# Performance work log

Hardware: AMD Instinct MI355X
Metric: run time of the kernel (lower is better)

The kernel has to match this reference:

```python
import jax, jax.numpy as jnp
import numpy as np

NUM_HEADS = 4

def setup_inputs() -> dict:
    key = jax.random.key(0)
    k1, k2, k3, k4 = jax.random.split(key, 4)
    B, N, D = 8, 768, 2048
    x = jax.random.normal(k1, (B, N, D), dtype=jnp.float32)
    s = 1.0 / np.sqrt(N)
    W_qk = jax.random.normal(k2, (N, N), dtype=jnp.float32) * s
    W_v = jax.random.normal(k3, (N, N), dtype=jnp.float32) * s
    W_out = jax.random.normal(k4, (N, N), dtype=jnp.float32) * s
    return {"x": x, "W_qk": W_qk, "W_v": W_v, "W_out": W_out}

def reference(x, W_qk, W_v, W_out):
    B, N, D = x.shape
    H = NUM_HEADS
    n = N // H
    y = jnp.swapaxes(x, 1, 2)                    # (B, D, N): attention over channels D
    qk = y @ W_qk.T                              # (B, D, N)
    v = y @ W_v.T                                # (B, D, N)
    # to heads: (B, D, N) -> (B, H, D, n)
    qk = jnp.swapaxes(qk.reshape(B, D, H, n), 1, 2)
    v = jnp.swapaxes(v.reshape(B, D, H, n), 1, 2)
    dot = jnp.einsum('bhdn,bhen->bhde', qk, qk)  # (B, H, D, D)
    q2 = jnp.sum(qk * qk, axis=-1)               # (B, H, D)
    # negative squared Euclidean distance logits: 2*q.k - ||q||^2 - ||k||^2
    logits = 2.0 * dot - q2[..., :, None] - q2[..., None, :]
    attn = jax.nn.softmax(logits, axis=-1)
    w = jnp.einsum('bhde,bhen->bhdn', attn, v)   # (B, H, D, n)
    # from heads: (B, H, D, n) -> (B, D, N)
    w = jnp.swapaxes(w, 1, 2).reshape(B, D, N)
    out = w @ W_out.T                            # (B, D, N)
    return jnp.swapaxes(out, 1, 2)               # (B, N, D)
```

## Files before the change

### kernel.cpp

```cpp
#include <hip/hip_runtime.h>
#include <stdint.h>

#define B_  8
#define N_  768
#define D_  2048
#define H_  4
#define HN  192

#define QROW 200
#define VROW 72
#define KTILE_B 25600
#define VTILE_B 27648

#define LOG2E 1.4426950408889634f
#define C2    2.8853901617f

typedef unsigned short u16;
typedef float    f32x4 __attribute__((ext_vector_type(4)));
typedef __bf16   bf16x8 __attribute__((ext_vector_type(8)));
typedef __bf16   bf16x4 __attribute__((ext_vector_type(4)));
typedef uint32_t u32x4 __attribute__((ext_vector_type(4)));
typedef uint32_t u32x2 __attribute__((ext_vector_type(2)));

__device__ __forceinline__ u16 f2bf(float f) {
  return __builtin_bit_cast(u16, (__bf16)f);
}

typedef const __attribute__((address_space(1))) void* gas_ptr;
typedef __attribute__((address_space(3))) void* las_ptr;
__device__ __forceinline__ void gld16(const void* g, void* l) {
  __builtin_amdgcn_global_load_lds((gas_ptr)g, (las_ptr)l, 16, 0, 0);
}

__global__ __launch_bounds__(256) void transpose_x(const float* __restrict__ x,
                                                   u16* __restrict__ xt) {
  __shared__ float tile[64][65];
  const int d0 = blockIdx.x * 64;
  const int n0 = blockIdx.y * 64;
  const int b  = blockIdx.z;
  const int t   = threadIdx.x;
  const int col = t & 63;
  const int rb  = (t >> 6) * 16;
  const float* src = x + ((size_t)b * N_ + n0) * D_ + d0;
  #pragma unroll
  for (int i = 0; i < 16; i++)
    tile[rb + i][col] = src[(size_t)(rb + i) * D_ + col];
  __syncthreads();
  u16* dst = xt + ((size_t)b * D_ + d0) * N_ + n0;
  #pragma unroll
  for (int i = 0; i < 16; i++)
    dst[(size_t)(rb + i) * N_ + col] = f2bf(tile[col][rb + i]);
}

__global__ __launch_bounds__(256) void cvt_w(const float* __restrict__ a,
                                             const float* __restrict__ b,
                                             const float* __restrict__ c,
                                             u16* __restrict__ oa,
                                             u16* __restrict__ ob,
                                             u16* __restrict__ oc) {
  const float* src = (blockIdx.y == 0) ? a : ((blockIdx.y == 1) ? b : c);
  u16*         dst = (blockIdx.y == 0) ? oa : ((blockIdx.y == 1) ? ob : oc);
  const int i = (blockIdx.x * 256 + threadIdx.x) * 4;
  f32x4 v = *(const f32x4*)(src + i);
  u16 tmp[4];
  #pragma unroll
  for (int j = 0; j < 4; j++) tmp[j] = f2bf(v[j]);
  *(u32x2*)(dst + i) = *(u32x2*)tmp;
}

__global__ __launch_bounds__(256) void zero_q2(float* __restrict__ q2) {
  q2[blockIdx.x * 256 + threadIdx.x] = 0.f;
}

__global__ __launch_bounds__(256, 2) void qkv_gemm(const u16* __restrict__ xt,
                                                   const u16* __restrict__ wqk,
                                                   const u16* __restrict__ wv,
                                                   u16* __restrict__ qkb,
                                                   u16* __restrict__ vtb,
                                                   float* __restrict__ q2) {
  const int b     = blockIdx.z;
  const int dtile = blockIdx.x;
  const int d0    = dtile * 128;
  const int j0    = blockIdx.y * 128;
  const int tid  = threadIdx.x;
  const int wave = tid >> 6, lane = tid & 63;
  const int l15  = lane & 15, quad = lane >> 4;
  const int wm = wave >> 1, wn = wave & 1;

  __shared__ u16 At[128 * 32];
  __shared__ u16 Bq[128 * 32];
  __shared__ u16 Bv[128 * 32];

  const f32x4 fz = {0.f, 0.f, 0.f, 0.f};
  f32x4 accq[4][4];
  f32x4 accv[4][4];
  #pragma unroll
  for (int i = 0; i < 4; i++)
    #pragma unroll
    for (int j = 0; j < 4; j++) { accq[i][j] = fz; accv[i][j] = fz; }

  const int srow  = tid >> 2;
  const int sbyte = (tid & 3) * 16;
  const u16* ax = xt  + ((size_t)b * D_ + d0 + srow) * N_;
  const u16* bq = wqk + (size_t)(j0 + srow) * N_;
  const u16* bv = wv  + (size_t)(j0 + srow) * N_;

  for (int k0 = 0; k0 < N_; k0 += 32) {
    __syncthreads();
    #pragma unroll
    for (int c = 0; c < 2; c++) {
      gld16((const char*)(ax + (size_t)c * 64 * N_ + k0) + sbyte,
            (char*)At + c * 4096 + tid * 16);
      gld16((const char*)(bq + (size_t)c * 64 * N_ + k0) + sbyte,
            (char*)Bq + c * 4096 + tid * 16);
      gld16((const char*)(bv + (size_t)c * 64 * N_ + k0) + sbyte,
            (char*)Bv + c * 4096 + tid * 16);
    }
    __syncthreads();

    bf16x8 Af[4];
    #pragma unroll
    for (int mi = 0; mi < 4; mi++)
      Af[mi] = *(const bf16x8*)&At[(wm * 64 + mi * 16 + l15) * 32 + quad * 8];
    #pragma unroll
    for (int ni = 0; ni < 4; ni++) {
      bf16x8 Bqf = *(const bf16x8*)&Bq[(wn * 64 + ni * 16 + l15) * 32 + quad * 8];
      bf16x8 Bvf = *(const bf16x8*)&Bv[(wn * 64 + ni * 16 + l15) * 32 + quad * 8];
      #pragma unroll
      for (int mi = 0; mi < 4; mi++) {
        accq[ni][mi] = __builtin_amdgcn_mfma_f32_16x16x32_bf16(Bqf, Af[mi], accq[ni][mi], 0, 0, 0);
        accv[mi][ni] = __builtin_amdgcn_mfma_f32_16x16x32_bf16(Af[mi], Bvf, accv[mi][ni], 0, 0, 0);
      }
    }
  }

  const int h_w  = (j0 + wn * 64) / HN;
  const int jn_w = (j0 + wn * 64) % HN;
  const size_t bh = (size_t)b * H_ + h_w;

  #pragma unroll
  for (int md = 0; md < 4; md++) {
    float s = 0.f;
    #pragma unroll
    for (int nj = 0; nj < 4; nj++)
      #pragma unroll
      for (int r = 0; r < 4; r++) { float v = accq[nj][md][r]; s += v * v; }
    s += __shfl_xor(s, 16, 64);
    s += __shfl_xor(s, 32, 64);
    if (quad == 0)
      atomicAdd(&q2[bh * D_ + d0 + wm * 64 + md * 16 + l15], s * LOG2E);
  }

  u16* qtbase = qkb + bh * (size_t)(D_ * QROW);
  #pragma unroll
  for (int md = 0; md < 4; md++) {
    const size_t dro = (size_t)(d0 + wm * 64 + md * 16 + l15) * QROW;
    #pragma unroll
    for (int nj = 0; nj < 4; nj++) {
      bf16x4 tmp;
      #pragma unroll
      for (int r = 0; r < 4; r++) tmp[r] = (__bf16)accq[nj][md][r];
      *(bf16x4*)(qtbase + dro + jn_w + nj * 16 + quad * 4) = tmp;
    }
  }

  const int etile = dtile * 2 + wm;
  u16* vtbase = vtb + bh * (size_t)(32 * HN * VROW) + (size_t)etile * (HN * VROW);
  #pragma unroll
  for (int ni = 0; ni < 4; ni++) {
    const size_t jro = (size_t)(jn_w + ni * 16 + l15) * VROW;
    #pragma unroll
    for (int mi = 0; mi < 4; mi++) {
      bf16x4 tmp;
      #pragma unroll
      for (int r = 0; r < 4; r++) tmp[r] = (__bf16)accv[mi][ni][r];
      *(bf16x4*)(vtbase + jro + mi * 16 + quad * 4) = tmp;
    }
  }
}

__global__ __launch_bounds__(256, 2) void attn_kernel(const u16* __restrict__ qkb,
                                                      const u16* __restrict__ vtb,
                                                      const float* __restrict__ q2,
                                                      u16* __restrict__ wbuf) {
  const int bid  = blockIdx.x;
  const int bh   = (bid & 7) * 4 + (bid >> 7);
  const int dblk = (bid >> 3) & 15;
  const int b = bh >> 2, h = bh & 3;
  const int tid  = threadIdx.x;
  const int wave = tid >> 6, lane = tid & 63;
  const int l15  = lane & 15, quad = lane >> 4;

  __shared__ u16 Klds[64 * QROW];
  __shared__ u16 Vlds[HN * VROW];
  __shared__ u16 Plds[4][32][VROW];

  const u16* kg = qkb + (size_t)bh * (D_ * QROW);
  const u16* vg = vtb + (size_t)bh * (32 * HN * VROW);
  const float* q2g = q2 + (size_t)bh * D_;

  bf16x8 Qf[2][6];
  {
    const u16* qrow = kg + (size_t)(dblk * 128 + wave * 32 + l15) * QROW + quad * 8;
    #pragma unroll
    for (int nt = 0; nt < 2; nt++)
      #pragma unroll
      for (int f = 0; f < 6; f++)
        Qf[nt][f] = *(const bf16x8*)(qrow + (size_t)nt * 16 * QROW + f * 32);
  }
  float cd[2];
  cd[0] = q2g[dblk * 128 + wave * 32 + l15];
  cd[1] = q2g[dblk * 128 + wave * 32 + 16 + l15];

  bf16x8 OnesF;
  #pragma unroll
  for (int j = 0; j < 8; j++) OnesF[j] = (__bf16)1.0f;

  const f32x4 fz = {0.f, 0.f, 0.f, 0.f};
  f32x4 O[2][12];
  f32x4 Or[2];
  #pragma unroll
  for (int mt = 0; mt < 2; mt++) {
    Or[mt] = fz;
    #pragma unroll
    for (int c = 0; c < 12; c++) O[mt][c] = fz;
  }

  for (int t = 0; t < 32; t++) {
    __syncthreads();
    {
      const char* ks = (const char*)kg + (size_t)t * KTILE_B;
      char* kd = (char*)Klds;
      for (int c = wave; c < 25; c += 4)
        gld16(ks + c * 1024 + lane * 16, kd + c * 1024 + lane * 16);
      const char* vs = (const char*)vg + (size_t)t * VTILE_B;
      char* vd = (char*)Vlds;
      for (int c = wave; c < 27; c += 4)
        gld16(vs + c * 1024 + lane * 16, vd + c * 1024 + lane * 16);
    }
    __syncthreads();

    #pragma unroll
    for (int et = 0; et < 4; et++) {
      bf16x8 Kf[6];
      #pragma unroll
      for (int f = 0; f < 6; f++)
        Kf[f] = *(const bf16x8*)&Klds[(et * 16 + l15) * QROW + f * 32 + quad * 8];
      f32x4 S0 = fz, S1 = fz;
      __builtin_amdgcn_s_setprio(1);
      #pragma unroll
      for (int f = 0; f < 6; f++) {
        S0 = __builtin_amdgcn_mfma_f32_16x16x32_bf16(Kf[f], Qf[0][f], S0, 0, 0, 0);
        S1 = __builtin_amdgcn_mfma_f32_16x16x32_bf16(Kf[f], Qf[1][f], S1, 0, 0, 0);
      }
      __builtin_amdgcn_s_setprio(0);
      const f32x4 ce = *(const f32x4*)&q2g[t * 64 + et * 16 + quad * 4];
      bf16x4 pb0, pb1;
      #pragma unroll
      for (int r = 0; r < 4; r++) {
        float p0 = __builtin_amdgcn_exp2f(__builtin_fmaf(S0[r], C2, -(ce[r] + cd[0])));
        float p1 = __builtin_amdgcn_exp2f(__builtin_fmaf(S1[r], C2, -(ce[r] + cd[1])));
        pb0[r] = (__bf16)p0;
        pb1[r] = (__bf16)p1;
      }
      *(bf16x4*)&Plds[wave][l15][et * 16 + quad * 4]      = pb0;
      *(bf16x4*)&Plds[wave][16 + l15][et * 16 + quad * 4] = pb1;
    }

    #pragma unroll
    for (int kk = 0; kk < 2; kk++) {
      bf16x8 Pf0 = *(const bf16x8*)&Plds[wave][l15][kk * 32 + quad * 8];
      bf16x8 Pf1 = *(const bf16x8*)&Plds[wave][16 + l15][kk * 32 + quad * 8];
      __builtin_amdgcn_s_setprio(1);
      #pragma unroll
      for (int c = 0; c < 12; c++) {
        bf16x8 Vf = *(const bf16x8*)&Vlds[(c * 16 + l15) * VROW + kk * 32 + quad * 8];
        O[0][c] = __builtin_amdgcn_mfma_f32_16x16x32_bf16(Pf0, Vf, O[0][c], 0, 0, 0);
        O[1][c] = __builtin_amdgcn_mfma_f32_16x16x32_bf16(Pf1, Vf, O[1][c], 0, 0, 0);
      }
      Or[0] = __builtin_amdgcn_mfma_f32_16x16x32_bf16(Pf0, OnesF, Or[0], 0, 0, 0);
      Or[1] = __builtin_amdgcn_mfma_f32_16x16x32_bf16(Pf1, OnesF, Or[1], 0, 0, 0);
      __builtin_amdgcn_s_setprio(0);
    }
  }

  #pragma unroll
  for (int mt = 0; mt < 2; mt++)
    #pragma unroll
    for (int r = 0; r < 4; r++) {
      const float inv = __builtin_amdgcn_rcpf(Or[mt][r]);
      const int d = dblk * 128 + wave * 32 + mt * 16 + quad * 4 + r;
      u16* wrow = wbuf + ((size_t)b * D_ + d) * N_ + h * HN;
      #pragma unroll
      for (int c = 0; c < 12; c++)
        wrow[c * 16 + l15] = f2bf(O[mt][c][r] * inv);
    }
}

__global__ __launch_bounds__(256, 2) void out_gemm(const u16* __restrict__ wbuf,
                                                   const u16* __restrict__ wout,
                                                   float* __restrict__ outp) {
  const int b  = blockIdx.z;
  const int d0 = blockIdx.x * 128;
  const int i0 = blockIdx.y * 128;
  const int tid  = threadIdx.x;
  const int wave = tid >> 6, lane = tid & 63;
  const int l15  = lane & 15, quad = lane >> 4;
  const int wm = wave >> 1, wn = wave & 1;

  __shared__ u16 At[128 * 32];
  __shared__ u16 Bt[128 * 32];

  const f32x4 fz = {0.f, 0.f, 0.f, 0.f};
  f32x4 acc[4][4];
  #pragma unroll
  for (int i = 0; i < 4; i++)
    #pragma unroll
    for (int j = 0; j < 4; j++) acc[i][j] = fz;

  const int srow  = tid >> 2;
  const int sbyte = (tid & 3) * 16;
  const u16* ax = wbuf + ((size_t)b * D_ + d0 + srow) * N_;
  const u16* bw = wout + (size_t)(i0 + srow) * N_;

  for (int k0 = 0; k0 < N_; k0 += 32) {
    __syncthreads();
    #pragma unroll
    for (int c = 0; c < 2; c++) {
      gld16((const char*)(ax + (size_t)c * 64 * N_ + k0) + sbyte,
            (char*)At + c * 4096 + tid * 16);
      gld16((const char*)(bw + (size_t)c * 64 * N_ + k0) + sbyte,
            (char*)Bt + c * 4096 + tid * 16);
    }
    __syncthreads();

    bf16x8 Af[4];
    #pragma unroll
    for (int mi = 0; mi < 4; mi++)
      Af[mi] = *(const bf16x8*)&At[(wm * 64 + mi * 16 + l15) * 32 + quad * 8];
    #pragma unroll
    for (int ni = 0; ni < 4; ni++) {
      bf16x8 Bf = *(const bf16x8*)&Bt[(wn * 64 + ni * 16 + l15) * 32 + quad * 8];
      #pragma unroll
      for (int mi = 0; mi < 4; mi++)
        acc[mi][ni] = __builtin_amdgcn_mfma_f32_16x16x32_bf16(Af[mi], Bf, acc[mi][ni], 0, 0, 0);
    }
  }

  #pragma unroll
  for (int ni = 0; ni < 4; ni++) {
    float* orow = outp + ((size_t)b * N_ + i0 + wn * 64 + ni * 16 + l15) * D_
                + d0 + wm * 64 + quad * 4;
    #pragma unroll
    for (int mi = 0; mi < 4; mi++)
      *(f32x4*)(orow + mi * 16) = acc[mi][ni];
  }
}

extern "C" void kernel_launch(void* const* d_in, const int* in_sizes, int n_in,
                              void* d_out, int out_size, void* d_ws, size_t ws_size,
                              hipStream_t stream) {
  (void)in_sizes; (void)n_in; (void)out_size; (void)ws_size;
  const float* x    = (const float*)d_in[0];
  const float* Wqk  = (const float*)d_in[1];
  const float* Wv   = (const float*)d_in[2];
  const float* Wout = (const float*)d_in[3];
  float* outp = (float*)d_out;

  char* ws = (char*)d_ws;
  size_t off = 0;
  u16* xt   = (u16*)(ws + off); off += (size_t)B_ * D_ * N_ * 2;
  u16* qkb  = (u16*)(ws + off); off += (size_t)B_ * H_ * D_ * QROW * 2;
  u16* vtb  = (u16*)(ws + off); off += (size_t)B_ * H_ * 32 * HN * VROW * 2;
  float* q2 = (float*)(ws + off); off += (size_t)B_ * H_ * D_ * 4;
  u16* wqk_bf  = (u16*)(ws + off); off += (size_t)N_ * N_ * 2;
  u16* wv_bf   = (u16*)(ws + off); off += (size_t)N_ * N_ * 2;
  u16* wout_bf = (u16*)(ws + off); off += (size_t)N_ * N_ * 2;
  u16* wbuf = xt;

  transpose_x<<<dim3(D_ / 64, N_ / 64, B_), 256, 0, stream>>>(x, xt);
  cvt_w<<<dim3((N_ * N_) / (256 * 4), 3), 256, 0, stream>>>(Wqk, Wv, Wout, wqk_bf, wv_bf, wout_bf);
  zero_q2<<<dim3((B_ * H_ * D_) / 256), 256, 0, stream>>>(q2);
  qkv_gemm<<<dim3(D_ / 128, N_ / 128, B_), 256, 0, stream>>>(xt, wqk_bf, wv_bf, qkb, vtb, q2);
  attn_kernel<<<dim3((D_ / 128) * B_ * H_), 256, 0, stream>>>(qkb, vtb, q2, wbuf);
  out_gemm<<<dim3(D_ / 128, N_ / 128, B_), 256, 0, stream>>>(wbuf, wout_bf, outp);
}
```

Baseline: 298.9 us.

## Prefetch next K/V tile into registers in attention and merge prep kernels

The attention kernel previously loaded each K/V tile straight into LDS and waited on it before computing. It now loads the next tile into registers (13 x 16B per thread) during the current tile's compute, then writes it to LDS after a barrier, so global latency overlaps the MFMA work. The transpose, weight-conversion and q2-zeroing kernels are also merged into one launch to cut launch overhead. The register staging adds about 52 VGPRs per thread on top of a large accumulator set, which may cut occupancy or cause spills.

```diff
diff --git a/kernel.cpp b/kernel.cpp
--- a/kernel.cpp
+++ b/kernel.cpp
@@ -11,6 +11,8 @@
 #define VROW 72
 #define KTILE_B 25600
 #define VTILE_B 27648
+#define KV_CHUNKS 3328
+#define K_CHUNKS  1600
 
 #define LOG2E 1.4426950408889634f
 #define C2    2.8853901617f
@@ -32,44 +34,49 @@
   __builtin_amdgcn_global_load_lds((gas_ptr)g, (las_ptr)l, 16, 0, 0);
 }
 
-__global__ __launch_bounds__(256) void transpose_x(const float* __restrict__ x,
-                                                   u16* __restrict__ xt) {
+__global__ __launch_bounds__(256) void prep(const float* __restrict__ x,
+                                            const float* __restrict__ Wqk,
+                                            const float* __restrict__ Wv,
+                                            const float* __restrict__ Wout,
+                                            u16* __restrict__ xt,
+                                            u16* __restrict__ oqk,
+                                            u16* __restrict__ ov,
+                                            u16* __restrict__ oout,
+                                            float* __restrict__ q2) {
   __shared__ float tile[64][65];
-  const int d0 = blockIdx.x * 64;
-  const int n0 = blockIdx.y * 64;
-  const int b  = blockIdx.z;
+  const int bid = blockIdx.x;
   const int t   = threadIdx.x;
-  const int col = t & 63;
-  const int rb  = (t >> 6) * 16;
-  const float* src = x + ((size_t)b * N_ + n0) * D_ + d0;
-  #pragma unroll
-  for (int i = 0; i < 16; i++)
-    tile[rb + i][col] = src[(size_t)(rb + i) * D_ + col];
-  __syncthreads();
-  u16* dst = xt + ((size_t)b * D_ + d0) * N_ + n0;
-  #pragma unroll
-  for (int i = 0; i < 16; i++)
-    dst[(size_t)(rb + i) * N_ + col] = f2bf(tile[col][rb + i]);
-}
-
-__global__ __launch_bounds__(256) void cvt_w(const float* __restrict__ a,
-                                             const float* __restrict__ b,
-                                             const float* __restrict__ c,
-                                             u16* __restrict__ oa,
-                                             u16* __restrict__ ob,
-                                             u16* __restrict__ oc) {
-  const float* src = (blockIdx.y == 0) ? a : ((blockIdx.y == 1) ? b : c);
-  u16*         dst = (blockIdx.y == 0) ? oa : ((blockIdx.y == 1) ? ob : oc);
-  const int i = (blockIdx.x * 256 + threadIdx.x) * 4;
-  f32x4 v = *(const f32x4*)(src + i);
-  u16 tmp[4];
-  #pragma unroll
-  for (int j = 0; j < 4; j++) tmp[j] = f2bf(v[j]);
-  *(u32x2*)(dst + i) = *(u32x2*)tmp;
-}
-
-__global__ __launch_bounds__(256) void zero_q2(float* __restrict__ q2) {
-  q2[blockIdx.x * 256 + threadIdx.x] = 0.f;
+  if (bid < 3072) {
+    const int d0 = (bid & 31) * 64;
+    const int n0 = ((bid >> 5) % 12) * 64;
+    const int b  = (bid >> 5) / 12;
+    const int col = t & 63;
+    const int rb  = (t >> 6) * 16;
+    const float* src = x + ((size_t)b * N_ + n0) * D_ + d0;
+    #pragma unroll
+    for (int i = 0; i < 16; i++)
+      tile[rb + i][col] = src[(size_t)(rb + i) * D_ + col];
+    __syncthreads();
+    u16* dst = xt + ((size_t)b * D_ + d0) * N_ + n0;
+    #pragma unroll
+    for (int i = 0; i < 16; i++)
+      dst[(size_t)(rb + i) * N_ + col] = f2bf(tile[col][rb + i]);
+  } else if (bid < 4800) {
+    const int r   = bid - 3072;
+    const int mat = r / 576;
+    const float* src = (mat == 0) ? Wqk : ((mat == 1) ? Wv : Wout);
+    u16*         dst = (mat == 0) ? oqk : ((mat == 1) ? ov : oout);
+    const int i = ((r % 576) * 256 + t) * 4;
+    f32x4 v = *(const f32x4*)(src + i);
+    bf16x4 tmp;
+    #pragma unroll
+    for (int j = 0; j < 4; j++) tmp[j] = (__bf16)v[j];
+    *(bf16x4*)(dst + i) = tmp;
+  } else {
+    const f32x4 fz = {0.f, 0.f, 0.f, 0.f};
+    const int i = ((bid - 4800) * 256 + t) * 4;
+    *(f32x4*)(q2 + i) = fz;
+  }
 }
 
 __global__ __launch_bounds__(256, 2) void qkv_gemm(const u16* __restrict__ xt,
@@ -191,9 +198,10 @@
   const int wave = tid >> 6, lane = tid & 63;
   const int l15  = lane & 15, quad = lane >> 4;
 
-  __shared__ u16 Klds[64 * QROW];
-  __shared__ u16 Vlds[HN * VROW];
+  __shared__ u16 KV[(KTILE_B + VTILE_B) / 2];
   __shared__ u16 Plds[4][32][VROW];
+  u16* Klds = KV;
+  u16* Vlds = KV + KTILE_B / 2;
 
   const u16* kg = qkb + (size_t)bh * (D_ * QROW);
   const u16* vg = vtb + (size_t)bh * (32 * HN * VROW);
@@ -226,19 +234,29 @@
     for (int c = 0; c < 12; c++) O[mt][c] = fz;
   }
 
+  u32x4 stg[13];
+  #define LOADT(T)                                                            \
+    {                                                                         \
+      const char* kgt = (const char*)kg + (size_t)(T) * KTILE_B;              \
+      const char* vgt = (const char*)vg + (size_t)(T) * VTILE_B;              \
+      _Pragma("unroll")                                                       \
+      for (int i = 0; i < 13; i++) {                                          \
+        const int c = tid + 256 * i;                                          \
+        const char* src = (c < K_CHUNKS) ? (kgt + (size_t)c * 16)             \
+                                         : (vgt + (size_t)(c - K_CHUNKS) * 16); \
+        stg[i] = *(const u32x4*)src;                                          \
+      }                                                                       \
+    }
+
+  LOADT(0);
+
   for (int t = 0; t < 32; t++) {
     __syncthreads();
-    {
-      const char* ks = (const char*)kg + (size_t)t * KTILE_B;
-      char* kd = (char*)Klds;
-      for (int c = wave; c < 25; c += 4)
-        gld16(ks + c * 1024 + lane * 16, kd + c * 1024 + lane * 16);
-      const char* vs = (const char*)vg + (size_t)t * VTILE_B;
-      char* vd = (char*)Vlds;
-      for (int c = wave; c < 27; c += 4)
-        gld16(vs + c * 1024 + lane * 16, vd + c * 1024 + lane * 16);
-    }
-    __syncthreads();
+    #pragma unroll
+    for (int i = 0; i < 13; i++)
+      *(u32x4*)((char*)KV + (size_t)(tid + 256 * i) * 16) = stg[i];
+    __syncthreads();
+    if (t < 31) LOADT(t + 1);
 
     #pragma unroll
     for (int et = 0; et < 4; et++) {
@@ -378,9 +396,7 @@
   u16* wout_bf = (u16*)(ws + off); off += (size_t)N_ * N_ * 2;
   u16* wbuf = xt;
 
-  transpose_x<<<dim3(D_ / 64, N_ / 64, B_), 256, 0, stream>>>(x, xt);
-  cvt_w<<<dim3((N_ * N_) / (256 * 4), 3), 256, 0, stream>>>(Wqk, Wv, Wout, wqk_bf, wv_bf, wout_bf);
-  zero_q2<<<dim3((B_ * H_ * D_) / 256), 256, 0, stream>>>(q2);
+  prep<<<dim3(4864), 256, 0, stream>>>(x, Wqk, Wv, Wout, xt, wqk_bf, wv_bf, wout_bf, q2);
   qkv_gemm<<<dim3(D_ / 128, N_ / 128, B_), 256, 0, stream>>>(xt, wqk_bf, wv_bf, qkb, vtb, q2);
   attn_kernel<<<dim3((D_ / 128) * B_ * H_), 256, 0, stream>>>(qkb, vtb, q2, wbuf);
   out_gemm<<<dim3(D_ / 128, N_ / 128, B_), 256, 0, stream>>>(wbuf, wout_bf, outp);
```

Result: slower. 335.4 us (+12.2%).
